# Performance work log

Hardware: AMD Instinct MI355X
Metric: run time of the kernel (lower is better)

## Reference

```python
import jax, jax.numpy as jnp
import numpy as np

EPS = 1e-5  # BatchNorm2d default eps


def _resize_bilinear(x, out_h, out_w):
    # PyTorch F.interpolate(mode='bilinear', align_corners=False, antialias=False):
    # input coord = (out + 0.5)/scale - 0.5  ->  translation = 0.5*(scale-1)
    b, c, h, w = x.shape
    sh, sw = out_h / h, out_w / w
    scale = jnp.array([sh, sw], dtype=jnp.float32)
    trans = jnp.array([0.5 * (sh - 1.0), 0.5 * (sw - 1.0)], dtype=jnp.float32)
    return jax.image.scale_and_translate(
        x, (b, c, out_h, out_w), (2, 3), scale, trans,
        method='linear', antialias=False)


def setup_inputs() -> dict:
    key = jax.random.key(0)
    ks = jax.random.split(key, 6)
    B, C, IC, H, W = 4, 64, 16, 128, 128
    init = lambda k, shape, fan_in: (
        jax.random.normal(k, shape, jnp.float32) / np.float32(np.sqrt(fan_in)))
    return {
        'x': jax.random.normal(ks[0], (B, C, H, W), jnp.float32),
        'g_w': init(ks[1], (IC, C), C), 'g_b': jnp.zeros((IC,), jnp.float32),
        'theta_w': init(ks[2], (IC, C), C), 'theta_b': jnp.zeros((IC,), jnp.float32),
        'phi_w': init(ks[3], (IC, C), C), 'phi_b': jnp.zeros((IC,), jnp.float32),
        'out_w': init(ks[4], (C, IC), IC), 'out_b': jnp.zeros((C,), jnp.float32),
        'bn_gamma': jnp.ones((C,), jnp.float32), 'bn_beta': jnp.zeros((C,), jnp.float32),
    }


def reference(x, g_w, g_b, theta_w, theta_b, phi_w, phi_b,
              out_w, out_b, bn_gamma, bn_beta):
    b, c, h, w = x.shape
    dh, dw = h // 2, w // 2          # downsample_factor = 0.5
    xd = _resize_bilinear(x, dh, dw).reshape(b, c, dh * dw)  # [b,C,N]

    # 1x1 convs == per-pixel linear projections
    g_x = jnp.einsum('bcn,oc->bno', xd, g_w) + g_b          # [b,N,IC]
    th = jnp.einsum('bcn,oc->bno', xd, theta_w) + theta_b   # [b,N,IC]
    ph = jnp.einsum('bcn,oc->bon', xd, phi_w) + phi_b[None, :, None]  # [b,IC,N]

    f = jnp.einsum('bni,bim->bnm', th, ph)   # [b,N,N] score matrix (no scaling)
    attn = jax.nn.softmax(f, axis=-1)
    y = jnp.einsum('bnm,bmi->bni', attn, g_x)               # [b,N,IC]
    y = y.transpose(0, 2, 1).reshape(b, -1, dh, dw)         # [b,IC,dh,dw]

    y = _resize_bilinear(y, h, w)                            # upsample back
    y = jnp.einsum('bihw,ci->bchw', y, out_w) + out_b[None, :, None, None]

    z = x + y
    # BatchNorm2d in (default) training mode: biased batch stats over (B,H,W)
    mean = jnp.mean(z, axis=(0, 2, 3))
    var = jnp.var(z, axis=(0, 2, 3))
    zn = (z - mean[None, :, None, None]) * jax.lax.rsqrt(var + EPS)[None, :, None, None]
    return zn * bn_gamma[None, :, None, None] + bn_beta[None, :, None, None]
```

## Files before the change

kernel.cpp:

```cpp
#include <hip/hip_runtime.h>
#include <math.h>

#define NB 4
#define NC 64
#define NI 16
#define NH 128
#define NW 128
#define ND 64
#define NN 4096
#define KSPL 4

#define LOG2E 1.4426950408889634f

using bfrag = __attribute__((ext_vector_type(8))) short;
using ffrag = __attribute__((ext_vector_type(4))) float;

#if __has_builtin(__builtin_amdgcn_exp2f)
#define EXP2(x) __builtin_amdgcn_exp2f(x)
#else
#define EXP2(x) exp2f(x)
#endif

__device__ __forceinline__ unsigned bf16rne(float f) {
    unsigned u = __float_as_uint(f);
    return (u + 0x7FFFu + ((u >> 16) & 1u)) >> 16;
}
__device__ __forceinline__ unsigned pk_rne(float lo, float hi) {
    return bf16rne(lo) | (bf16rne(hi) << 16);
}
__device__ __forceinline__ unsigned pk_trunc(float lo, float hi) {
    return (__float_as_uint(lo) >> 16) | (__float_as_uint(hi) & 0xFFFF0000u);
}

extern "C" __global__ __launch_bounds__(256)
void k_proj(const float* __restrict__ x,
            const float* __restrict__ gw, const float* __restrict__ gb,
            const float* __restrict__ tw, const float* __restrict__ tb,
            const float* __restrict__ pw, const float* __restrict__ pb,
            uint4* __restrict__ th_sw, uint4* __restrict__ phi_sw,
            uint4* __restrict__ g_sw, float* __restrict__ stats)
{
    __shared__ float swt[NC][48];
    __shared__ float sb[48];
    __shared__ __align__(16) unsigned short gtile[16][256];
    int tid = threadIdx.x;
    if (blockIdx.x == 0 && tid < 128) stats[tid] = 0.f;
    for (int idx = tid; idx < NI*NC; idx += 256) {
        int o = idx >> 6, c = idx & 63;
        swt[c][o]      = tw[idx];
        swt[c][16 + o] = pw[idx];
        swt[c][32 + o] = gw[idx];
    }
    if (tid < 16) { sb[tid] = tb[tid]; sb[16+tid] = pb[tid]; sb[32+tid] = gb[tid]; }
    __syncthreads();

    int bq = blockIdx.x * 256 + tid;
    int b = bq >> 12, q = bq & 4095;
    int i = q >> 6, j = q & 63;
    const float* xp = x + (((size_t)(b*NC)*NH + (2*i+1))*NW + (2*j+1));
    float aT[16], aP[16], aG[16];
#pragma unroll
    for (int o = 0; o < 16; ++o) { aT[o] = 0.f; aP[o] = 0.f; aG[o] = 0.f; }
    for (int c = 0; c < NC; ++c) {
        float xd = xp[(size_t)c*NH*NW];
        const float* wr = swt[c];
#pragma unroll
        for (int o = 0; o < 16; ++o) aT[o] += xd*wr[o];
#pragma unroll
        for (int o = 0; o < 16; ++o) aP[o] += xd*wr[16+o];
#pragma unroll
        for (int o = 0; o < 16; ++o) aG[o] += xd*wr[32+o];
    }
#pragma unroll
    for (int o = 0; o < 16; ++o) {
        aT[o] = (aT[o] + sb[o]) * LOG2E;
        aP[o] =  aP[o] + sb[16+o];
        aG[o] =  aG[o] + sb[32+o];
    }

    const uint4 z4 = make_uint4(0u, 0u, 0u, 0u);
    {
        int n = q & 15;
        size_t base = (size_t)(bq >> 4) * 64;
        uint4 v0 = make_uint4(pk_rne(aT[0],aT[1]),  pk_rne(aT[2],aT[3]),
                              pk_rne(aT[4],aT[5]),  pk_rne(aT[6],aT[7]));
        uint4 v1 = make_uint4(pk_rne(aT[8],aT[9]),  pk_rne(aT[10],aT[11]),
                              pk_rne(aT[12],aT[13]),pk_rne(aT[14],aT[15]));
        th_sw[base +      n] = v0;
        th_sw[base + 16 + n] = v1;
        th_sw[base + 32 + n] = z4;
        th_sw[base + 48 + n] = z4;
    }
    {
        int w = q & 31;
        int gsel = (w >> 2) & 1;
        int r = ((w >> 3) << 2) | (w & 3);
        size_t kgroup = (size_t)b*256 + ((q >> 5) << 1) + gsel;
        size_t base = kgroup * 64;
        uint4 v0 = make_uint4(pk_rne(aP[0],aP[1]),  pk_rne(aP[2],aP[3]),
                              pk_rne(aP[4],aP[5]),  pk_rne(aP[6],aP[7]));
        uint4 v1 = make_uint4(pk_rne(aP[8],aP[9]),  pk_rne(aP[10],aP[11]),
                              pk_rne(aP[12],aP[13]),pk_rne(aP[14],aP[15]));
        phi_sw[base +      r] = v0;
        phi_sw[base + 16 + r] = v1;
        phi_sw[base + 32 + r] = z4;
        phi_sw[base + 48 + r] = z4;
    }
#pragma unroll
    for (int o = 0; o < 16; ++o) gtile[o][tid] = (unsigned short)bf16rne(aG[o]);
    __syncthreads();
    size_t gchunk0 = (size_t)b*128 + (size_t)(blockIdx.x & 15) * 8;
    for (int e = tid; e < 512; e += 256) {
        int c = e >> 6, L = e & 63, q8 = (L >> 4), n = L & 15;
        const uint4* src = (const uint4*)&gtile[n][c*32 + q8*8];
        g_sw[(gchunk0 + c)*64 + L] = *src;
    }
}

extern "C" __global__ __launch_bounds__(256)
void k_attn(const uint4* __restrict__ th_sw, const uint4* __restrict__ phi_sw,
            const uint4* __restrict__ g_sw, float* __restrict__ accp,
            float* __restrict__ lp)
{
    __shared__ uint4 sphi[16*64];
    __shared__ uint4 sg[8*64];
    __shared__ float sl[4][16];

    int tid = threadIdx.x;
    int wave = tid >> 6, lane = tid & 63;
    int quad = lane >> 4, low = lane & 15;
    int qgroup = blockIdx.x, ks = blockIdx.y, b = blockIdx.z;

    const bfrag* thF = (const bfrag*)th_sw;
    bfrag theta = thF[((size_t)b*256 + qgroup*4 + wave)*64 + lane];

    ffrag yacc = {0.f, 0.f, 0.f, 0.f};
    const ffrag zf = {0.f, 0.f, 0.f, 0.f};
    float lacc = 0.f;

    for (int chunk = 0; chunk < 4; ++chunk) {
        __syncthreads();
        const uint4* srcP = phi_sw + ((size_t)b*256 + ks*64 + chunk*16)*64;
        const uint4* srcG = g_sw   + ((size_t)b*128 + ks*32 + chunk*8 )*64;
#pragma unroll
        for (int it = 0; it < 4; ++it) sphi[it*256 + tid] = srcP[it*256 + tid];
#pragma unroll
        for (int it = 0; it < 2; ++it) sg[it*256 + tid]   = srcG[it*256 + tid];
        __syncthreads();

        const bfrag* sphiF = (const bfrag*)sphi;
        const bfrag* sgF   = (const bfrag*)sg;
#pragma unroll
        for (int s = 0; s < 8; ++s) {
            bfrag pA = sphiF[(s*2+0)*64 + lane];
            bfrag pB = sphiF[(s*2+1)*64 + lane];
            bfrag vf = sgF[s*64 + lane];
            ffrag sA = __builtin_amdgcn_mfma_f32_16x16x32_bf16(pA, theta, zf, 0, 0, 0);
            ffrag sB = __builtin_amdgcn_mfma_f32_16x16x32_bf16(pB, theta, zf, 0, 0, 0);
            float eA0 = EXP2(sA[0]), eA1 = EXP2(sA[1]), eA2 = EXP2(sA[2]), eA3 = EXP2(sA[3]);
            float eB0 = EXP2(sB[0]), eB1 = EXP2(sB[1]), eB2 = EXP2(sB[2]), eB3 = EXP2(sB[3]);
            lacc += ((eA0+eA1) + (eA2+eA3)) + ((eB0+eB1) + (eB2+eB3));
            union { unsigned u[4]; bfrag f; } pu;
            pu.u[0] = pk_trunc(eA0, eA1);
            pu.u[1] = pk_trunc(eA2, eA3);
            pu.u[2] = pk_trunc(eB0, eB1);
            pu.u[3] = pk_trunc(eB2, eB3);
            yacc = __builtin_amdgcn_mfma_f32_16x16x32_bf16(pu.f, vf, yacc, 0, 0, 0);
        }
    }

    lacc += __shfl_xor(lacc, 16, 64);
    lacc += __shfl_xor(lacc, 32, 64);
    if (lane < 16) sl[wave][lane] = lacc;
    __syncthreads();

    int qbase = qgroup*64 + wave*16;
    size_t pbase = ((size_t)ks*NB + b)*NN;
#pragma unroll
    for (int reg = 0; reg < 4; ++reg) {
        int qq = qbase + quad*4 + reg;
        accp[(pbase + qq)*16 + low] = yacc[reg];
    }
    if (lane < 16) lp[pbase + qbase + lane] = lacc;
}

extern "C" __global__ __launch_bounds__(256)
void k_combine(const float* __restrict__ accp, const float* __restrict__ lp,
               float* __restrict__ yt)
{
    int bq = blockIdx.x*256 + threadIdx.x;
    int b = bq >> 12, q = bq & 4095;
    float acc[16];
#pragma unroll
    for (int k = 0; k < 16; ++k) acc[k] = 0.f;
    float l = 0.f;
    for (int s = 0; s < KSPL; ++s) {
        const float4* ap = (const float4*)accp + (((size_t)s*NB + b)*NN + q)*4;
        float4 v0 = ap[0], v1 = ap[1], v2 = ap[2], v3 = ap[3];
        acc[0]+=v0.x;  acc[1]+=v0.y;  acc[2]+=v0.z;  acc[3]+=v0.w;
        acc[4]+=v1.x;  acc[5]+=v1.y;  acc[6]+=v1.z;  acc[7]+=v1.w;
        acc[8]+=v2.x;  acc[9]+=v2.y;  acc[10]+=v2.z; acc[11]+=v2.w;
        acc[12]+=v3.x; acc[13]+=v3.y; acc[14]+=v3.z; acc[15]+=v3.w;
        l += lp[((size_t)s*NB + b)*NN + q];
    }
    float inv = 1.f / l;
#pragma unroll
    for (int i = 0; i < 16; ++i)
        yt[((size_t)b*NI + i)*NN + q] = acc[i]*inv;
}

extern "C" __global__ __launch_bounds__(128)
void k_out(const float* __restrict__ yt, const float* __restrict__ x,
           const float* __restrict__ ow, const float* __restrict__ ob,
           float* __restrict__ z)
{
    __shared__ float syup[NI][NW];
    __shared__ float sw[NC*NI];
    __shared__ float sbv[NC];
    int w = threadIdx.x, h = blockIdx.x, b = blockIdx.y;
    for (int idx = w; idx < NC*NI; idx += 128) sw[idx] = ow[idx];
    if (w < NC) sbv[w] = ob[w];

    float chf = h*0.5f - 0.5f;
    int h0 = (int)floorf(chf); float fh = chf - (float)h0;
    int h1 = h0 + 1; if (h1 > ND-1) h1 = ND-1; if (h0 < 0) h0 = 0;
    float cwf = w*0.5f - 0.5f;
    int w0 = (int)floorf(cwf); float fw = cwf - (float)w0;
    int w1 = w0 + 1; if (w1 > ND-1) w1 = ND-1; if (w0 < 0) w0 = 0;
    float w00=(1.f-fh)*(1.f-fw), w01=(1.f-fh)*fw, w10=fh*(1.f-fw), w11=fh*fw;
    for (int i = 0; i < NI; ++i) {
        const float* yp = yt + ((size_t)b*NI + i)*NN;
        syup[i][w] = w00*yp[h0*ND+w0] + w01*yp[h0*ND+w1]
                   + w10*yp[h1*ND+w0] + w11*yp[h1*ND+w1];
    }
    __syncthreads();

    float yv[16];
#pragma unroll
    for (int i = 0; i < 16; ++i) yv[i] = syup[i][w];
    for (int c = 0; c < NC; ++c) {
        const float* wr = sw + c*16;
        float acc = sbv[c];
#pragma unroll
        for (int i = 0; i < 16; ++i) acc += wr[i]*yv[i];
        size_t off = (((size_t)(b*NC + c))*NH + h)*NW + w;
        z[off] = x[off] + acc;
    }
}

extern "C" __global__ __launch_bounds__(256)
void k_stats(const float* __restrict__ z, float* __restrict__ stats)
{
    int c = blockIdx.x, b = blockIdx.y;
    const float4* zp = (const float4*)(z + ((size_t)(b*NC + c))*NH*NW);
    float s = 0.f, s2 = 0.f;
    for (int i = threadIdx.x; i < NH*NW/4; i += 256) {
        float4 v = zp[i];
        s  += v.x + v.y + v.z + v.w;
        s2 += v.x*v.x + v.y*v.y + v.z*v.z + v.w*v.w;
    }
#pragma unroll
    for (int off = 32; off > 0; off >>= 1) {
        s  += __shfl_down(s, off);
        s2 += __shfl_down(s2, off);
    }
    __shared__ float red[8];
    int lane = threadIdx.x & 63, wv = threadIdx.x >> 6;
    if (lane == 0) { red[wv] = s; red[4+wv] = s2; }
    __syncthreads();
    if (threadIdx.x == 0) {
        atomicAdd(&stats[c],    red[0]+red[1]+red[2]+red[3]);
        atomicAdd(&stats[NC+c], red[4]+red[5]+red[6]+red[7]);
    }
}

extern "C" __global__ __launch_bounds__(256)
void k_norm(const float* __restrict__ z, const float* __restrict__ stats,
            const float* __restrict__ gamma, const float* __restrict__ beta,
            float* __restrict__ out)
{
    size_t i4 = (size_t)blockIdx.x*256 + threadIdx.x;
    int c = (int)((i4 >> 12) & 63);
    const float inv_cnt = 1.f/65536.f;
    float mean = stats[c]*inv_cnt;
    float var  = stats[NC+c]*inv_cnt - mean*mean;
    float rs = rsqrtf(var + 1e-5f);
    float ga = gamma[c]*rs;
    float be = beta[c] - mean*ga;
    float4 v = ((const float4*)z)[i4];
    ((float4*)out)[i4] = make_float4(v.x*ga+be, v.y*ga+be, v.z*ga+be, v.w*ga+be);
}

extern "C" void kernel_launch(void* const* d_in, const int* in_sizes, int n_in,
                              void* d_out, int out_size, void* d_ws, size_t ws_size,
                              hipStream_t stream)
{
    const float* x     = (const float*)d_in[0];
    const float* gw    = (const float*)d_in[1];
    const float* gb    = (const float*)d_in[2];
    const float* tw    = (const float*)d_in[3];
    const float* tb    = (const float*)d_in[4];
    const float* pw    = (const float*)d_in[5];
    const float* pb    = (const float*)d_in[6];
    const float* ow    = (const float*)d_in[7];
    const float* ob    = (const float*)d_in[8];
    const float* gamma = (const float*)d_in[9];
    const float* beta  = (const float*)d_in[10];
    float* out = (float*)d_out;

    char* wsb = (char*)d_ws;
    uint4* th_sw  = (uint4*)(wsb);
    uint4* phi_sw = (uint4*)(wsb + (1u<<20));
    uint4* g_sw   = (uint4*)(wsb + (2u<<20));
    float* yt     = (float*)(wsb + (2u<<20) + (512u<<10));
    float* lp     = (float*)(wsb + (3u<<20) + (512u<<10));
    float* stats  = (float*)(wsb + (3u<<20) + (768u<<10));
    char*  big    =          wsb + (3u<<20) + (769u<<10);
    float* accp   = (float*)big;
    float* z      = (float*)big;

    k_proj   <<<64, 256, 0, stream>>>(x, gw, gb, tw, tb, pw, pb,
                                      th_sw, phi_sw, g_sw, stats);
    k_attn   <<<dim3(64, KSPL, NB), 256, 0, stream>>>(th_sw, phi_sw, g_sw, accp, lp);
    k_combine<<<64, 256, 0, stream>>>(accp, lp, yt);
    k_out    <<<dim3(NH, NB), 128, 0, stream>>>(yt, x, ow, ob, z);
    k_stats  <<<dim3(NC, NB), 256, 0, stream>>>(z, stats);
    k_norm   <<<4096, 256, 0, stream>>>(z, stats, gamma, beta, out);
}
```

Before: 151.2 us.

## Split projection over channels, use K16 MFMA for scores, fuse combine into output

k_proj now launches 256 blocks, each covering one downsampled row. Its four waves split the 64 input channels and reduce partial sums through shared memory, which raises parallelism over the old 64-block launch. The theta and phi buffers drop their zero padding and use the 16x16x16 bf16 MFMA, which halves score MFMA work and load traffic. The combine kernel is fused into the upsample/output-projection kernel with a specialized 2x bilinear stencil, removing the yt round trip and one launch. Risks are the extra shared-memory reduction cost and that the new layouts must match exactly.

```diff
diff --git a/kernel.cpp b/kernel.cpp
--- a/kernel.cpp
+++ b/kernel.cpp
@@ -12,8 +12,9 @@
 
 #define LOG2E 1.4426950408889634f
 
-using bfrag = __attribute__((ext_vector_type(8))) short;
-using ffrag = __attribute__((ext_vector_type(4))) float;
+using bfrag  = __attribute__((ext_vector_type(8))) short;
+using bfrag4 = __attribute__((ext_vector_type(4))) short;
+using ffrag  = __attribute__((ext_vector_type(4))) float;
 
 #if __has_builtin(__builtin_amdgcn_exp2f)
 #define EXP2(x) __builtin_amdgcn_exp2f(x)
@@ -32,18 +33,32 @@
     return (__float_as_uint(lo) >> 16) | (__float_as_uint(hi) & 0xFFFF0000u);
 }
 
+__device__ __forceinline__ ffrag mfma_qk(bfrag4 a, bfrag4 b, ffrag c) {
+#if __has_builtin(__builtin_amdgcn_mfma_f32_16x16x16bf16_1k)
+    return __builtin_amdgcn_mfma_f32_16x16x16bf16_1k(a, b, c, 0, 0, 0);
+#else
+    union { bfrag4 h[2]; bfrag v; } ua, ub;
+    bfrag4 zz = {0, 0, 0, 0};
+    ua.h[0] = a; ua.h[1] = zz;
+    ub.h[0] = b; ub.h[1] = zz;
+    return __builtin_amdgcn_mfma_f32_16x16x32_bf16(ua.v, ub.v, c, 0, 0, 0);
+#endif
+}
+
 extern "C" __global__ __launch_bounds__(256)
 void k_proj(const float* __restrict__ x,
             const float* __restrict__ gw, const float* __restrict__ gb,
             const float* __restrict__ tw, const float* __restrict__ tb,
             const float* __restrict__ pw, const float* __restrict__ pb,
-            uint4* __restrict__ th_sw, uint4* __restrict__ phi_sw,
+            uint2* __restrict__ th_sw, uint2* __restrict__ phi_sw,
             uint4* __restrict__ g_sw, float* __restrict__ stats)
 {
     __shared__ float swt[NC][48];
     __shared__ float sb[48];
-    __shared__ __align__(16) unsigned short gtile[16][256];
+    __shared__ float red[3][64][49];
+    __shared__ __align__(16) unsigned short gtile[16][64];
     int tid = threadIdx.x;
+    int b = blockIdx.x >> 6, i = blockIdx.x & 63;
     if (blockIdx.x == 0 && tid < 128) stats[tid] = 0.f;
     for (int idx = tid; idx < NI*NC; idx += 256) {
         int o = idx >> 6, c = idx & 63;
@@ -54,85 +69,75 @@
     if (tid < 16) { sb[tid] = tb[tid]; sb[16+tid] = pb[tid]; sb[32+tid] = gb[tid]; }
     __syncthreads();
 
-    int bq = blockIdx.x * 256 + tid;
-    int b = bq >> 12, q = bq & 4095;
-    int i = q >> 6, j = q & 63;
-    const float* xp = x + (((size_t)(b*NC)*NH + (2*i+1))*NW + (2*j+1));
-    float aT[16], aP[16], aG[16];
-#pragma unroll
-    for (int o = 0; o < 16; ++o) { aT[o] = 0.f; aP[o] = 0.f; aG[o] = 0.f; }
-    for (int c = 0; c < NC; ++c) {
-        float xd = xp[(size_t)c*NH*NW];
-        const float* wr = swt[c];
-#pragma unroll
-        for (int o = 0; o < 16; ++o) aT[o] += xd*wr[o];
-#pragma unroll
-        for (int o = 0; o < 16; ++o) aP[o] += xd*wr[16+o];
-#pragma unroll
-        for (int o = 0; o < 16; ++o) aG[o] += xd*wr[32+o];
-    }
-#pragma unroll
-    for (int o = 0; o < 16; ++o) {
-        aT[o] = (aT[o] + sb[o]) * LOG2E;
-        aP[o] =  aP[o] + sb[16+o];
-        aG[o] =  aG[o] + sb[32+o];
-    }
-
-    const uint4 z4 = make_uint4(0u, 0u, 0u, 0u);
-    {
-        int n = q & 15;
-        size_t base = (size_t)(bq >> 4) * 64;
-        uint4 v0 = make_uint4(pk_rne(aT[0],aT[1]),  pk_rne(aT[2],aT[3]),
-                              pk_rne(aT[4],aT[5]),  pk_rne(aT[6],aT[7]));
-        uint4 v1 = make_uint4(pk_rne(aT[8],aT[9]),  pk_rne(aT[10],aT[11]),
-                              pk_rne(aT[12],aT[13]),pk_rne(aT[14],aT[15]));
-        th_sw[base +      n] = v0;
-        th_sw[base + 16 + n] = v1;
-        th_sw[base + 32 + n] = z4;
-        th_sw[base + 48 + n] = z4;
-    }
-    {
-        int w = q & 31;
-        int gsel = (w >> 2) & 1;
-        int r = ((w >> 3) << 2) | (w & 3);
-        size_t kgroup = (size_t)b*256 + ((q >> 5) << 1) + gsel;
-        size_t base = kgroup * 64;
-        uint4 v0 = make_uint4(pk_rne(aP[0],aP[1]),  pk_rne(aP[2],aP[3]),
-                              pk_rne(aP[4],aP[5]),  pk_rne(aP[6],aP[7]));
-        uint4 v1 = make_uint4(pk_rne(aP[8],aP[9]),  pk_rne(aP[10],aP[11]),
-                              pk_rne(aP[12],aP[13]),pk_rne(aP[14],aP[15]));
-        phi_sw[base +      r] = v0;
-        phi_sw[base + 16 + r] = v1;
-        phi_sw[base + 32 + r] = z4;
-        phi_sw[base + 48 + r] = z4;
-    }
-#pragma unroll
-    for (int o = 0; o < 16; ++o) gtile[o][tid] = (unsigned short)bf16rne(aG[o]);
-    __syncthreads();
-    size_t gchunk0 = (size_t)b*128 + (size_t)(blockIdx.x & 15) * 8;
-    for (int e = tid; e < 512; e += 256) {
-        int c = e >> 6, L = e & 63, q8 = (L >> 4), n = L & 15;
-        const uint4* src = (const uint4*)&gtile[n][c*32 + q8*8];
-        g_sw[(gchunk0 + c)*64 + L] = *src;
-    }
-}
-
-extern "C" __global__ __launch_bounds__(256)
-void k_attn(const uint4* __restrict__ th_sw, const uint4* __restrict__ phi_sw,
+    int j = tid & 63, part = tid >> 6;
+    const float* xp = x + (((size_t)(b*NC + part*16))*NH + (2*i+1))*NW + (2*j+1);
+    float a[48];
+#pragma unroll
+    for (int k = 0; k < 48; ++k) a[k] = 0.f;
+    for (int cc = 0; cc < 16; ++cc) {
+        float xd = xp[(size_t)cc*NH*NW];
+        const float* wr = swt[part*16 + cc];
+#pragma unroll
+        for (int k = 0; k < 48; ++k) a[k] += xd*wr[k];
+    }
+    if (part != 0) {
+#pragma unroll
+        for (int k = 0; k < 48; ++k) red[part-1][j][k] = a[k];
+    }
+    __syncthreads();
+    if (part == 0) {
+        float aT[16], aP[16], aG[16];
+#pragma unroll
+        for (int o = 0; o < 16; ++o) {
+            float vT = a[o]    + red[0][j][o]    + red[1][j][o]    + red[2][j][o];
+            float vP = a[16+o] + red[0][j][16+o] + red[1][j][16+o] + red[2][j][16+o];
+            float vG = a[32+o] + red[0][j][32+o] + red[1][j][32+o] + red[2][j][32+o];
+            aT[o] = (vT + sb[o]) * LOG2E;
+            aP[o] =  vP + sb[16+o];
+            aG[o] =  vG + sb[32+o];
+        }
+        int q = i*64 + j;
+        int n = j & 15;
+        size_t qtile = (size_t)b*256 + (q >> 4);
+#pragma unroll
+        for (int qd = 0; qd < 4; ++qd)
+            th_sw[qtile*64 + qd*16 + n] =
+                make_uint2(pk_rne(aT[4*qd], aT[4*qd+1]), pk_rne(aT[4*qd+2], aT[4*qd+3]));
+        int wk = j & 31;
+        int f = (wk >> 2) & 1;
+        int r = ((wk >> 3) << 2) | (wk & 3);
+        size_t kgrp = (size_t)b*256 + (q >> 5)*2 + f;
+#pragma unroll
+        for (int qd = 0; qd < 4; ++qd)
+            phi_sw[kgrp*64 + qd*16 + r] =
+                make_uint2(pk_rne(aP[4*qd], aP[4*qd+1]), pk_rne(aP[4*qd+2], aP[4*qd+3]));
+#pragma unroll
+        for (int o = 0; o < 16; ++o) gtile[o][j] = (unsigned short)bf16rne(aG[o]);
+    }
+    __syncthreads();
+    if (tid < 128) {
+        int c2 = tid >> 6, L = tid & 63;
+        int n = L & 15, q8 = L >> 4;
+        const uint4* src = (const uint4*)&gtile[n][c2*32 + q8*8];
+        g_sw[((size_t)b*128 + i*2 + c2)*64 + L] = *src;
+    }
+}
+
+extern "C" __global__ __launch_bounds__(256, 4)
+void k_attn(const uint2* __restrict__ th_sw, const uint2* __restrict__ phi_sw,
             const uint4* __restrict__ g_sw, float* __restrict__ accp,
             float* __restrict__ lp)
 {
-    __shared__ uint4 sphi[16*64];
-    __shared__ uint4 sg[8*64];
-    __shared__ float sl[4][16];
-
+    __shared__ __align__(16) uint2 sphi[16*64];
+    __shared__ __align__(16) uint4 sg[8*64];
     int tid = threadIdx.x;
     int wave = tid >> 6, lane = tid & 63;
     int quad = lane >> 4, low = lane & 15;
     int qgroup = blockIdx.x, ks = blockIdx.y, b = blockIdx.z;
 
-    const bfrag* thF = (const bfrag*)th_sw;
-    bfrag theta = thF[((size_t)b*256 + qgroup*4 + wave)*64 + lane];
+    union { uint2 u; bfrag4 f; } thu;
+    thu.u = th_sw[((size_t)b*256 + qgroup*4 + wave)*64 + lane];
+    bfrag4 theta = thu.f;
 
     ffrag yacc = {0.f, 0.f, 0.f, 0.f};
     const ffrag zf = {0.f, 0.f, 0.f, 0.f};
@@ -140,23 +145,23 @@
 
     for (int chunk = 0; chunk < 4; ++chunk) {
         __syncthreads();
-        const uint4* srcP = phi_sw + ((size_t)b*256 + ks*64 + chunk*16)*64;
-        const uint4* srcG = g_sw   + ((size_t)b*128 + ks*32 + chunk*8 )*64;
-#pragma unroll
-        for (int it = 0; it < 4; ++it) sphi[it*256 + tid] = srcP[it*256 + tid];
-#pragma unroll
-        for (int it = 0; it < 2; ++it) sg[it*256 + tid]   = srcG[it*256 + tid];
+        const uint4* srcP = (const uint4*)(phi_sw + ((size_t)b*256 + ks*64 + chunk*16)*64);
+        const uint4* srcG = g_sw + ((size_t)b*128 + ks*32 + chunk*8)*64;
+        ((uint4*)sphi)[tid]       = srcP[tid];
+        ((uint4*)sphi)[256 + tid] = srcP[256 + tid];
+        sg[tid]       = srcG[tid];
+        sg[256 + tid] = srcG[256 + tid];
         __syncthreads();
 
-        const bfrag* sphiF = (const bfrag*)sphi;
-        const bfrag* sgF   = (const bfrag*)sg;
+        const bfrag4* sphiF = (const bfrag4*)sphi;
+        const bfrag*  sgF   = (const bfrag*)sg;
 #pragma unroll
         for (int s = 0; s < 8; ++s) {
-            bfrag pA = sphiF[(s*2+0)*64 + lane];
-            bfrag pB = sphiF[(s*2+1)*64 + lane];
-            bfrag vf = sgF[s*64 + lane];
-            ffrag sA = __builtin_amdgcn_mfma_f32_16x16x32_bf16(pA, theta, zf, 0, 0, 0);
-            ffrag sB = __builtin_amdgcn_mfma_f32_16x16x32_bf16(pB, theta, zf, 0, 0, 0);
+            bfrag4 pA = sphiF[(2*s+0)*64 + lane];
+            bfrag4 pB = sphiF[(2*s+1)*64 + lane];
+            bfrag  vf = sgF[s*64 + lane];
+            ffrag sA = mfma_qk(pA, theta, zf);
+            ffrag sB = mfma_qk(pB, theta, zf);
             float eA0 = EXP2(sA[0]), eA1 = EXP2(sA[1]), eA2 = EXP2(sA[2]), eA3 = EXP2(sA[3]);
             float eB0 = EXP2(sB[0]), eB1 = EXP2(sB[1]), eB2 = EXP2(sB[2]), eB3 = EXP2(sB[3]);
             lacc += ((eA0+eA1) + (eA2+eA3)) + ((eB0+eB1) + (eB2+eB3));
@@ -171,80 +176,74 @@
 
     lacc += __shfl_xor(lacc, 16, 64);
     lacc += __shfl_xor(lacc, 32, 64);
-    if (lane < 16) sl[wave][lane] = lacc;
-    __syncthreads();
 
     int qbase = qgroup*64 + wave*16;
     size_t pbase = ((size_t)ks*NB + b)*NN;
 #pragma unroll
-    for (int reg = 0; reg < 4; ++reg) {
-        int qq = qbase + quad*4 + reg;
-        accp[(pbase + qq)*16 + low] = yacc[reg];
-    }
+    for (int reg = 0; reg < 4; ++reg)
+        accp[(pbase + qbase + quad*4 + reg)*16 + low] = yacc[reg];
     if (lane < 16) lp[pbase + qbase + lane] = lacc;
 }
 
 extern "C" __global__ __launch_bounds__(256)
-void k_combine(const float* __restrict__ accp, const float* __restrict__ lp,
-               float* __restrict__ yt)
-{
-    int bq = blockIdx.x*256 + threadIdx.x;
-    int b = bq >> 12, q = bq & 4095;
-    float acc[16];
-#pragma unroll
-    for (int k = 0; k < 16; ++k) acc[k] = 0.f;
-    float l = 0.f;
-    for (int s = 0; s < KSPL; ++s) {
-        const float4* ap = (const float4*)accp + (((size_t)s*NB + b)*NN + q)*4;
-        float4 v0 = ap[0], v1 = ap[1], v2 = ap[2], v3 = ap[3];
-        acc[0]+=v0.x;  acc[1]+=v0.y;  acc[2]+=v0.z;  acc[3]+=v0.w;
-        acc[4]+=v1.x;  acc[5]+=v1.y;  acc[6]+=v1.z;  acc[7]+=v1.w;
-        acc[8]+=v2.x;  acc[9]+=v2.y;  acc[10]+=v2.z; acc[11]+=v2.w;
-        acc[12]+=v3.x; acc[13]+=v3.y; acc[14]+=v3.z; acc[15]+=v3.w;
-        l += lp[((size_t)s*NB + b)*NN + q];
-    }
-    float inv = 1.f / l;
+void k_outz(const float* __restrict__ accp, const float* __restrict__ lp,
+            const float* __restrict__ x, const float* __restrict__ ow,
+            const float* __restrict__ ob, float* __restrict__ z)
+{
+    __shared__ float syd[2][NI][ND];
+    __shared__ float sl[2][ND];
+    __shared__ float swv[NC*NI];
+    __shared__ float sbv[NC];
+    int t = threadIdx.x;
+    int hp = blockIdx.x, b = blockIdx.y;
+    for (int idx = t; idx < NC*NI; idx += 256) swv[idx] = ow[idx];
+    if (t < NC) sbv[t] = ob[t];
+
+    {
+        int r = t >> 7, col = (t >> 1) & 63, half = t & 1;
+        int row = (r == 0) ? (hp > 0 ? hp-1 : 0) : hp;
+        int q = row*64 + col;
+        float4 a0 = make_float4(0.f,0.f,0.f,0.f), a1 = a0;
+        float lsum = 0.f;
+        for (int ks = 0; ks < KSPL; ++ks) {
+            const float4* ap = (const float4*)accp + (((size_t)ks*NB + b)*NN + q)*4 + 2*half;
+            float4 v0 = ap[0], v1 = ap[1];
+            a0.x += v0.x; a0.y += v0.y; a0.z += v0.z; a0.w += v0.w;
+            a1.x += v1.x; a1.y += v1.y; a1.z += v1.z; a1.w += v1.w;
+            if (half == 0) lsum += lp[((size_t)ks*NB + b)*NN + q];
+        }
+        if (half == 0) sl[r][col] = lsum;
+        __syncthreads();
+        float inv = 1.f / sl[r][col];
+        int i0 = 8*half;
+        syd[r][i0+0][col] = a0.x*inv; syd[r][i0+1][col] = a0.y*inv;
+        syd[r][i0+2][col] = a0.z*inv; syd[r][i0+3][col] = a0.w*inv;
+        syd[r][i0+4][col] = a1.x*inv; syd[r][i0+5][col] = a1.y*inv;
+        syd[r][i0+6][col] = a1.z*inv; syd[r][i0+7][col] = a1.w*inv;
+    }
+    __syncthreads();
+
+    int w = t & 127, hsel = t >> 7;
+    int h = 2*hp + hsel;
+    float wh0 = hsel ? 0.f : 0.5f;
+    float wh1 = hsel ? 1.f : 0.5f;
+    int c0, c1; float wc0, wc1;
+    if (w & 1) { c0 = c1 = (w-1) >> 1; wc0 = 1.f; wc1 = 0.f; }
+    else       { c1 = w >> 1; c0 = c1 ? c1-1 : 0; wc0 = 0.5f; wc1 = 0.5f; }
+    float yv[16];
 #pragma unroll
     for (int i = 0; i < 16; ++i)
-        yt[((size_t)b*NI + i)*NN + q] = acc[i]*inv;
-}
-
-extern "C" __global__ __launch_bounds__(128)
-void k_out(const float* __restrict__ yt, const float* __restrict__ x,
-           const float* __restrict__ ow, const float* __restrict__ ob,
-           float* __restrict__ z)
-{
-    __shared__ float syup[NI][NW];
-    __shared__ float sw[NC*NI];
-    __shared__ float sbv[NC];
-    int w = threadIdx.x, h = blockIdx.x, b = blockIdx.y;
-    for (int idx = w; idx < NC*NI; idx += 128) sw[idx] = ow[idx];
-    if (w < NC) sbv[w] = ob[w];
-
-    float chf = h*0.5f - 0.5f;
-    int h0 = (int)floorf(chf); float fh = chf - (float)h0;
-    int h1 = h0 + 1; if (h1 > ND-1) h1 = ND-1; if (h0 < 0) h0 = 0;
-    float cwf = w*0.5f - 0.5f;
-    int w0 = (int)floorf(cwf); float fw = cwf - (float)w0;
-    int w1 = w0 + 1; if (w1 > ND-1) w1 = ND-1; if (w0 < 0) w0 = 0;
-    float w00=(1.f-fh)*(1.f-fw), w01=(1.f-fh)*fw, w10=fh*(1.f-fw), w11=fh*fw;
-    for (int i = 0; i < NI; ++i) {
-        const float* yp = yt + ((size_t)b*NI + i)*NN;
-        syup[i][w] = w00*yp[h0*ND+w0] + w01*yp[h0*ND+w1]
-                   + w10*yp[h1*ND+w0] + w11*yp[h1*ND+w1];
-    }
-    __syncthreads();
-
-    float yv[16];
-#pragma unroll
-    for (int i = 0; i < 16; ++i) yv[i] = syup[i][w];
+        yv[i] = wh0*(wc0*syd[0][i][c0] + wc1*syd[0][i][c1])
+              + wh1*(wc0*syd[1][i][c0] + wc1*syd[1][i][c1]);
+
+    const float* xb = x + (((size_t)(b*NC))*NH + h)*NW + w;
+    float* zb       = z + (((size_t)(b*NC))*NH + h)*NW + w;
     for (int c = 0; c < NC; ++c) {
-        const float* wr = sw + c*16;
+        const float* wr = swv + c*16;
         float acc = sbv[c];
 #pragma unroll
         for (int i = 0; i < 16; ++i) acc += wr[i]*yv[i];
-        size_t off = (((size_t)(b*NC + c))*NH + h)*NW + w;
-        z[off] = x[off] + acc;
+        zb[(size_t)c*NH*NW] = xb[(size_t)c*NH*NW] + acc;
     }
 }
 
@@ -309,21 +308,18 @@
     float* out = (float*)d_out;
 
     char* wsb = (char*)d_ws;
-    uint4* th_sw  = (uint4*)(wsb);
-    uint4* phi_sw = (uint4*)(wsb + (1u<<20));
-    uint4* g_sw   = (uint4*)(wsb + (2u<<20));
-    float* yt     = (float*)(wsb + (2u<<20) + (512u<<10));
-    float* lp     = (float*)(wsb + (3u<<20) + (512u<<10));
-    float* stats  = (float*)(wsb + (3u<<20) + (768u<<10));
-    char*  big    =          wsb + (3u<<20) + (769u<<10);
-    float* accp   = (float*)big;
-    float* z      = (float*)big;
-
-    k_proj   <<<64, 256, 0, stream>>>(x, gw, gb, tw, tb, pw, pb,
-                                      th_sw, phi_sw, g_sw, stats);
-    k_attn   <<<dim3(64, KSPL, NB), 256, 0, stream>>>(th_sw, phi_sw, g_sw, accp, lp);
-    k_combine<<<64, 256, 0, stream>>>(accp, lp, yt);
-    k_out    <<<dim3(NH, NB), 128, 0, stream>>>(yt, x, ow, ob, z);
-    k_stats  <<<dim3(NC, NB), 256, 0, stream>>>(z, stats);
-    k_norm   <<<4096, 256, 0, stream>>>(z, stats, gamma, beta, out);
-}
+    uint2* th_sw  = (uint2*)(wsb);
+    uint2* phi_sw = (uint2*)(wsb + (512u<<10));
+    uint4* g_sw   = (uint4*)(wsb + (1024u<<10));
+    float* lp     = (float*)(wsb + (1536u<<10));
+    float* stats  = (float*)(wsb + (1792u<<10));
+    float* accp   = (float*)(wsb + (2048u<<10));
+    float* z      = (float*)(wsb + (6u<<20) + (256u<<10));
+
+    k_proj <<<256, 256, 0, stream>>>(x, gw, gb, tw, tb, pw, pb,
+                                     th_sw, phi_sw, g_sw, stats);
+    k_attn <<<dim3(64, KSPL, NB), 256, 0, stream>>>(th_sw, phi_sw, g_sw, accp, lp);
+    k_outz <<<dim3(64, NB), 256, 0, stream>>>(accp, lp, x, ow, ob, z);
+    k_stats<<<dim3(NC, NB), 256, 0, stream>>>(z, stats);
+    k_norm <<<4096, 256, 0, stream>>>(z, stats, gamma, beta, out);
+}
```

Measured after the change: 130.3 us. -13.8%, faster.
